# Performance work log

Hardware: AMD Instinct MI355X
Metric: run time of the kernel (lower is better)

The kernel has to match this reference:

```python
import jax, jax.numpy as jnp
import numpy as np

LENGTH = 128
BATCH = 256
MARGIN = 1.0
BONUS = 1000.0  # constraint bump applied to chart cells
NCELLS = LENGTH * (LENGTH + 1) // 2
NCONSTR = 8


def _offsets(length):
    off = np.zeros(length, dtype=np.int64)
    for lvl in range(1, length):
        off[lvl] = off[lvl - 1] + (length - (lvl - 1))
    return off

OFF = _offsets(LENGTH)


def _level_child_indices(length):
    # For each level: flat chart indices of left/right children, shape (L, N)
    idx = {}
    for level in range(1, length):
        L = length - level
        pos = np.arange(L)[:, None]
        n = np.arange(level)[None, :]
        l_idx = OFF[n] + pos                      # left child span (pos, width n)
        r_idx = OFF[level - 1 - n] + pos + n + 1  # right child span
        idx[level] = (jnp.asarray(l_idx), jnp.asarray(r_idx))
    return idx

IDX = _level_child_indices(LENGTH)


def _score_offsets(length):
    soff, acc = {}, 0
    for level in range(1, length):
        soff[level] = acc
        acc += (length - level) * level
    return soff, acc

SOFF, TOTAL = _score_offsets(LENGTH)


def setup_inputs():
    key = jax.random.key(0)
    k1, k2 = jax.random.split(key)
    scores = jax.random.normal(k1, (BATCH, TOTAL), dtype=jnp.float32)
    # constrained spans at level >= 1 (original skips level <= 0)
    constraint_pos = jax.random.randint(k2, (BATCH, NCONSTR), LENGTH, NCELLS, dtype=jnp.int32)
    return {"scores": scores, "constraint_pos": constraint_pos}


def _cky(scores, chart):
    # max-plus semiring inside DP, level by level over the triangular chart
    B = chart.shape[0]
    for level in range(1, LENGTH):
        L = LENGTH - level
        N = level
        l_idx, r_idx = IDX[level]
        ls = chart[:, l_idx]                                     # (B, L, N)
        rs = chart[:, r_idx]                                     # (B, L, N)
        xs = scores[:, SOFF[level]:SOFF[level] + L * N].reshape(B, L, N)
        best = jnp.max(ls + rs + xs, axis=2)                     # (B, L)
        off = int(OFF[level])
        chart = chart.at[:, off:off + L].add(best)
    return chart[:, -1]                                          # (B,) root scores


def reference(scores, constraint_pos):
    B = scores.shape[0]
    zero_chart = jnp.zeros((B, NCELLS), dtype=scores.dtype)
    rows = jnp.arange(B)[:, None]
    constr_chart = zero_chart.at[rows, constraint_pos].set(BONUS)
    subtract = jnp.full((B,), BONUS * constraint_pos.shape[1], dtype=scores.dtype)
    constr_s = _cky(scores, constr_chart) - subtract
    pred_s = _cky(scores, zero_chart)
    mask = (jnp.abs(pred_s - constr_s) >= 0.001).astype(scores.dtype)
    hinge = jnp.maximum(MARGIN + pred_s - constr_s, 0.0) * mask
    msum = mask.sum()
    return jnp.where(msum > 0.1, hinge.sum() / jnp.maximum(msum, 1.0), hinge.sum())
```

## Files before the change

kernel.cpp:

```cpp
#include <hip/hip_runtime.h>
#include <hip/hip_bf16.h>
#include <math.h>

#define LEN 128
#define NCELLS 8256
#define TOTAL 349504
#define NCONSTR 8
#define BONUS 1000.0f
#define NT 512

__device__ __host__ constexpr int OFFi(int n){ return (n*(257-n))>>1; }
constexpr int SOFFc(int l){ int s=0; for(int k=1;k<l;k++) s += (LEN-k)*k; return s; }

__device__ __forceinline__ void level_barrier(){
    __builtin_amdgcn_sched_barrier(0);
    asm volatile("s_waitcnt lgkmcnt(0)\n\ts_barrier" ::: "memory");
    __builtin_amdgcn_sched_barrier(0);
}

__device__ __forceinline__ float dpp_xor1_max(float v){
    int r = __builtin_amdgcn_update_dpp(0, __float_as_int(v), 0xB1, 0xF, 0xF, true);
    return fmaxf(v, __int_as_float(r));
}
__device__ __forceinline__ float dpp_xor2_max(float v){
    int r = __builtin_amdgcn_update_dpp(0, __float_as_int(v), 0x4E, 0xF, 0xF, true);
    return fmaxf(v, __int_as_float(r));
}
template<int LG>
__device__ __forceinline__ void redmax2(float& a, float& b){
    #pragma unroll
    for (int mm=(1<<LG)>>1; mm>=4; mm>>=1){
        a=fmaxf(a,__shfl_xor(a,mm));
        b=fmaxf(b,__shfl_xor(b,mm));
    }
    if constexpr (LG>=2){ a=dpp_xor2_max(a); b=dpp_xor2_max(b); }
    if constexpr (LG>=1){ a=dpp_xor1_max(a); b=dpp_xor1_max(b); }
}

__device__ __forceinline__ bool chit(int q, const int4 c0, const int4 c1){
    return (q==c0.x)|(q==c0.y)|(q==c0.z)|(q==c0.w)|
           (q==c1.x)|(q==c1.y)|(q==c1.z)|(q==c1.w);
}

template<int LVL, int LG, int LG2>
__device__ __forceinline__ void lstep(const float* __restrict__ g,
    float2* __restrict__ chart, float2 (&lv)[16],
    float (&xc)[16], float (&xn)[16],
    const int4 cc0, const int4 cc1, const int tid)
{
    constexpr int N = LVL, L = LEN - LVL;
    constexpr int T = 1<<LG;
    constexpr int JM = (N + T - 1)/T;
    const int pos = tid >> LG;
    const int sub = tid & (T-1);

    if constexpr (LVL < 127){
        constexpr int T2 = 1<<LG2;
        constexpr int N2 = LVL+1, L2 = LEN-LVL-1;
        constexpr int JM2 = (N2 + T2 - 1)/T2;
        constexpr int SO = SOFFc(LVL+1);
        const int pos2 = tid >> LG2;
        const int sub2 = tid & (T2-1);
        if (pos2 < L2){
            const float* __restrict__ gp = g + SO + pos2*N2 + sub2;
            #pragma unroll
            for (int j=0;j<JM2;j++)
                if (sub2 + j*T2 < N2) xn[j] = gp[j*T2];
        }
    }

    float2 rv[JM];
    if (pos < L){
        #pragma unroll
        for (int j=0;j<JM;j++){
            const int n = sub + j*T;
            const int ri = (n < N) ? (OFFi(N-1-n) + pos + n + 1) : 0;
            rv[j] = chart[ri];
        }
    }

    float bp = -INFINITY, bc = -INFINITY;
    if (pos < L){
        #pragma unroll
        for (int j=0;j<JM;j++){
            const int n = sub + j*T;
            const float x = (n < N) ? xc[j] : -INFINITY;
            bp = fmaxf(bp, lv[j].x + rv[j].x + x);
            bc = fmaxf(bc, lv[j].y + rv[j].y + x);
        }
    }
    redmax2<LG>(bp, bc);

    const int q = OFFi(N) + pos;
    const float bon = chit(q, cc0, cc1) ? BONUS : 0.f;
    const float2 cv = make_float2(bp, bc + bon);
    if (pos < L && sub == 0) chart[q] = cv;

    {
        constexpr int asub  = N & (T-1);
        constexpr int aslot = N >> LG;
        static_assert(aslot < 16, "slot overflow");
        if (sub == asub){ lv[aslot] = cv; }
    }

    level_barrier();
}

__device__ __forceinline__ void trans64(const float2* __restrict__ chart,
                                        float2 (&lv)[16], const int tid)
{
    const int pos = tid >> 3;
    const int sub = tid & 7;
    #pragma unroll
    for (int j=0;j<8;j++){
        const int n = sub + 8*j;
        lv[j] = chart[OFFi(n) + pos];
    }
}

template<int L>
__device__ __forceinline__ void runlv(const float* __restrict__ g,
    float2* __restrict__ chart, float2 (&lv)[16],
    float (&xc)[16], float (&xn)[16],
    const int4 cc0, const int4 cc1, const int tid)
{
    if constexpr (L <= 127){
        constexpr int LG  = (L < 64) ? 2 : 3;
        constexpr int LG2 = (L+1 < 64) ? 2 : 3;
        lstep<L, LG, LG2>(g, chart, lv, xc, xn, cc0, cc1, tid);
        if constexpr (L == 63) trans64(chart, lv, tid);
        runlv<L+1>(g, chart, lv, xn, xc, cc0, cc1, tid);
    }
}

__global__ __launch_bounds__(NT)
void cky_fused_kernel(const float* __restrict__ scores,
                      const int* __restrict__ cpos,
                      float* __restrict__ ws)
{
    __shared__ float2 chart[NCELLS];

    const int b   = blockIdx.x;
    const int tid = threadIdx.x;
    const float* __restrict__ g = scores + (size_t)b * TOTAL;

    const int4* __restrict__ cp4 = (const int4*)(cpos + b * NCONSTR);
    const int4 cc0 = cp4[0];
    const int4 cc1 = cp4[1];

    float  xA[16], xB[16];
    float2 lv[16];
    #pragma unroll
    for (int j=0;j<16;j++) lv[j] = make_float2(0.f, 0.f);

    {
        const int pos = tid>>2, sub = tid&3;
        if (sub==0 && pos<127) xA[0] = g[pos];
    }

    if (tid < 128) chart[tid] = make_float2(0.f, 0.f);
    level_barrier();

    runlv<1>(g, chart, lv, xA, xB, cc0, cc1, tid);

    if (tid == 0){
        const float2 f = chart[OFFi(127)];
        const float pred   = f.x;
        const float constr = f.y - BONUS * NCONSTR;
        const float diff   = pred - constr;
        const float mask   = (fabsf(diff) >= 0.001f) ? 1.f : 0.f;
        const float hinge  = fmaxf(1.0f + diff, 0.f) * mask;
        atomicAdd(ws + 0, hinge);
        atomicAdd(ws + 1, mask);
    }
}

__global__ void final_kernel(const float* __restrict__ ws, float* __restrict__ out){
    const float h = ws[0];
    const float m = ws[1];
    out[0] = (m > 0.1f) ? (h / fmaxf(m, 1.f)) : h;
}

extern "C" void kernel_launch(void* const* d_in, const int* in_sizes, int n_in,
                              void* d_out, int out_size, void* d_ws, size_t ws_size,
                              hipStream_t stream) {
    const float* scores = (const float*)d_in[0];
    const int*   cpos   = (const int*)d_in[1];
    float* out = (float*)d_out;
    float* ws  = (float*)d_ws;

    hipMemsetAsync(ws, 0, 2 * sizeof(float), stream);
    cky_fused_kernel<<<dim3(256), dim3(NT), 0, stream>>>(scores, cpos, ws);
    final_kernel<<<dim3(1), dim3(1), 0, stream>>>(ws, out);
}
```

Before: 148.1 us.

## Store chart by anti-diagonal and widen reduction groups at high levels

```diff
diff --git a/kernel.cpp b/kernel.cpp
--- a/kernel.cpp
+++ b/kernel.cpp
@@ -10,7 +10,9 @@
 #define NT 512
 
 __device__ __host__ constexpr int OFFi(int n){ return (n*(257-n))>>1; }
+__device__ __host__ constexpr int ADIAG(int d){ return (d*(d+1))>>1; }
 constexpr int SOFFc(int l){ int s=0; for(int k=1;k<l;k++) s += (LEN-k)*k; return s; }
+constexpr int lgfor(int l){ return l<64?2 : l<96?3 : l<112?4 : l<120?5 : 6; }
 
 __device__ __forceinline__ void level_barrier(){
     __builtin_amdgcn_sched_barrier(0);
@@ -49,41 +51,43 @@
     const int4 cc0, const int4 cc1, const int tid)
 {
     constexpr int N = LVL, L = LEN - LVL;
-    constexpr int T = 1<<LG;
-    constexpr int JM = (N + T - 1)/T;
+    constexpr int T = 1 << LG;
+    constexpr int JM = (N + T - 1) / T;
     const int pos = tid >> LG;
-    const int sub = tid & (T-1);
-
-    if constexpr (LVL < 127){
-        constexpr int T2 = 1<<LG2;
-        constexpr int N2 = LVL+1, L2 = LEN-LVL-1;
-        constexpr int JM2 = (N2 + T2 - 1)/T2;
-        constexpr int SO = SOFFc(LVL+1);
-        const int pos2 = tid >> LG2;
-        const int sub2 = tid & (T2-1);
+    const int sub = tid & (T - 1);
+
+    if constexpr (LG2 >= 0){
+        constexpr int T2 = 1 << LG2;
+        constexpr int N2 = LVL + 1, L2 = LEN - LVL - 1;
+        constexpr int JM2 = (N2 + T2 - 1) / T2;
+        constexpr int SO2 = SOFFc(LVL + 1);
+        const int pos2 = tid >> LG2, sub2 = tid & (T2 - 1);
         if (pos2 < L2){
-            const float* __restrict__ gp = g + SO + pos2*N2 + sub2;
+            const float* __restrict__ gp = g + SO2 + pos2 * N2 + sub2;
             #pragma unroll
-            for (int j=0;j<JM2;j++)
-                if (sub2 + j*T2 < N2) xn[j] = gp[j*T2];
+            for (int j = 0; j < JM2; j++)
+                if (sub2 + j * T2 < N2) xn[j] = gp[j * T2];
         }
     }
 
     float2 rv[JM];
-    if (pos < L){
+    {
+        const int pc   = (pos < L) ? pos : (L - 1);
+        const int d    = pc + N;
+        const int jml  = (N - sub + T - 1) >> LG;
+        const int base = ADIAG(d) + (N - 1) - sub;
         #pragma unroll
-        for (int j=0;j<JM;j++){
-            const int n = sub + j*T;
-            const int ri = (n < N) ? (OFFi(N-1-n) + pos + n + 1) : 0;
-            rv[j] = chart[ri];
+        for (int j = 0; j < JM; j++){
+            const int a = (j < jml) ? (base - j * T) : 0;
+            rv[j] = chart[a];
         }
     }
 
     float bp = -INFINITY, bc = -INFINITY;
     if (pos < L){
         #pragma unroll
-        for (int j=0;j<JM;j++){
-            const int n = sub + j*T;
+        for (int j = 0; j < JM; j++){
+            const int n = sub + j * T;
             const float x = (n < N) ? xc[j] : -INFINITY;
             bp = fmaxf(bp, lv[j].x + rv[j].x + x);
             bc = fmaxf(bc, lv[j].y + rv[j].y + x);
@@ -91,30 +95,35 @@
     }
     redmax2<LG>(bp, bc);
 
-    const int q = OFFi(N) + pos;
-    const float bon = chit(q, cc0, cc1) ? BONUS : 0.f;
-    const float2 cv = make_float2(bp, bc + bon);
-    if (pos < L && sub == 0) chart[q] = cv;
-
+    const int qrow = OFFi(N) + pos;
+    const float2 cv = make_float2(bp, bc + (chit(qrow, cc0, cc1) ? BONUS : 0.f));
+    if (pos < L && sub == 0){
+        const int d = pos + N;
+        chart[ADIAG(d) + N] = cv;
+    }
     {
-        constexpr int asub  = N & (T-1);
         constexpr int aslot = N >> LG;
+        constexpr int asub  = N & (T - 1);
         static_assert(aslot < 16, "slot overflow");
-        if (sub == asub){ lv[aslot] = cv; }
-    }
-
+        if (sub == asub) lv[aslot] = cv;
+    }
     level_barrier();
 }
 
-__device__ __forceinline__ void trans64(const float2* __restrict__ chart,
+template<int NEWLVL, int LGn>
+__device__ __forceinline__ void retrans(const float2* __restrict__ chart,
                                         float2 (&lv)[16], const int tid)
 {
-    const int pos = tid >> 3;
-    const int sub = tid & 7;
+    constexpr int Tn = 1 << LGn;
+    constexpr int JMn = (NEWLVL + Tn - 1) / Tn;
+    constexpr int Ln = LEN - NEWLVL;
+    const int p = tid >> LGn, s = tid & (Tn - 1);
+    const int pc = (p < Ln) ? p : (Ln - 1);
     #pragma unroll
-    for (int j=0;j<8;j++){
-        const int n = sub + 8*j;
-        lv[j] = chart[OFFi(n) + pos];
+    for (int j = 0; j < JMn; j++){
+        const int n  = s + j * Tn;
+        const int nn = (n < NEWLVL) ? n : 0;
+        lv[j] = chart[ADIAG(pc + nn) + nn];
     }
 }
 
@@ -125,11 +134,14 @@
     const int4 cc0, const int4 cc1, const int tid)
 {
     if constexpr (L <= 127){
-        constexpr int LG  = (L < 64) ? 2 : 3;
-        constexpr int LG2 = (L+1 < 64) ? 2 : 3;
+        constexpr int LG  = lgfor(L);
+        constexpr int LG2 = (L < 127) ? lgfor(L + 1) : -1;
         lstep<L, LG, LG2>(g, chart, lv, xc, xn, cc0, cc1, tid);
-        if constexpr (L == 63) trans64(chart, lv, tid);
-        runlv<L+1>(g, chart, lv, xn, xc, cc0, cc1, tid);
+        if constexpr (L == 63)  retrans<64, 3>(chart, lv, tid);
+        if constexpr (L == 95)  retrans<96, 4>(chart, lv, tid);
+        if constexpr (L == 111) retrans<112, 5>(chart, lv, tid);
+        if constexpr (L == 119) retrans<120, 6>(chart, lv, tid);
+        runlv<L + 1>(g, chart, lv, xn, xc, cc0, cc1, tid);
     }
 }
 
@@ -151,20 +163,20 @@
     float  xA[16], xB[16];
     float2 lv[16];
     #pragma unroll
-    for (int j=0;j<16;j++) lv[j] = make_float2(0.f, 0.f);
+    for (int j = 0; j < 16; j++) lv[j] = make_float2(0.f, 0.f);
 
     {
-        const int pos = tid>>2, sub = tid&3;
-        if (sub==0 && pos<127) xA[0] = g[pos];
-    }
-
-    if (tid < 128) chart[tid] = make_float2(0.f, 0.f);
+        const int pos = tid >> 2, sub = tid & 3;
+        if (sub == 0 && pos < 127) xA[0] = g[pos];
+    }
+
+    if (tid < 128) chart[ADIAG(tid)] = make_float2(0.f, 0.f);
     level_barrier();
 
     runlv<1>(g, chart, lv, xA, xB, cc0, cc1, tid);
 
     if (tid == 0){
-        const float2 f = chart[OFFi(127)];
+        const float2 f = chart[ADIAG(127) + 127];
         const float pred   = f.x;
         const float constr = f.y - BONUS * NCONSTR;
         const float diff   = pred - constr;
```

Result: no change. 147.8 us (-0.2%).
